# Optimization experiments

Measured on AMD Instinct MI355X. Metric: run time of the kernel, lower is better.

The kernel has to match this reference:

```python
import jax, jax.numpy as jnp
import numpy as np

N_NODES = 100000
N_EDGES = 1600000
IN, HID, OUT = 128, 128, 64


def setup_inputs() -> dict:
    key = jax.random.key(0)
    ks = jax.random.split(key, 12)
    x = jax.random.normal(ks[0], (N_NODES, IN), dtype=jnp.float32)
    src = jax.random.randint(ks[1], (N_EDGES,), 0, N_NODES, dtype=jnp.int32)
    dst = jax.random.randint(ks[2], (N_EDGES,), 0, N_NODES, dtype=jnp.int32)

    def lin(k, fan_in, fan_out):
        return jax.random.normal(k, (fan_in, fan_out), dtype=jnp.float32) / jnp.sqrt(jnp.float32(fan_in))

    return {
        "x": x, "src": src, "dst": dst,
        "w_self_0": lin(ks[3], IN, HID), "w_neigh_0": lin(ks[4], IN, HID), "b_0": jnp.zeros((HID,), jnp.float32),
        "w_self_1": lin(ks[5], HID, HID), "w_neigh_1": lin(ks[6], HID, HID), "b_1": jnp.zeros((HID,), jnp.float32),
        "w_self_2": lin(ks[7], HID, OUT), "w_neigh_2": lin(ks[8], HID, OUT), "b_2": jnp.zeros((OUT,), jnp.float32),
    }


def reference(x, src, dst, w_self_0, w_neigh_0, b_0, w_self_1, w_neigh_1, b_1, w_self_2, w_neigh_2, b_2):
    n = x.shape[0]
    # in-degree per dst node; zero-degree nodes keep aggregated 0 (clamp avoids div-by-0)
    deg = jax.ops.segment_sum(jnp.ones_like(dst, dtype=x.dtype), dst, num_segments=n)
    inv_deg = (1.0 / jnp.maximum(deg, 1.0))[:, None]

    def sage_layer(h, w_s, w_n, b):
        # irregular gather of src features, segment-mean over dst
        agg = jax.ops.segment_sum(h[src], dst, num_segments=n) * inv_deg
        return h @ w_s + agg @ w_n + b

    h = jax.nn.relu(sage_layer(x, w_self_0, w_neigh_0, b_0))   # dropout = identity (eval)
    h = jax.nn.relu(sage_layer(h, w_self_1, w_neigh_1, b_1))
    return sage_layer(h, w_self_2, w_neigh_2, b_2)
```

## Files before the change

### kernel.cpp

```cpp
#include <hip/hip_runtime.h>


#define NN 100000
#define NE 1600000
#define BSH 7
#define BND 128
#define NB  782
#define NBLKS 256
#define EPB ((NE + NBLKS - 1) / NBLKS)
#define STOT (NB * NBLKS)
#define NSB ((STOT + 1023) / 1024)
#define GEMM_BLOCKS 1563

typedef __attribute__((ext_vector_type(8))) short short8;
typedef __attribute__((ext_vector_type(4))) float f32x4;
typedef unsigned int uint;
typedef unsigned short ushort;

__device__ inline ushort f2bf(float f) {
    uint u = __float_as_uint(f);
    u += 0x7FFFu + ((u >> 16) & 1u);
    return (ushort)(u >> 16);
}
__device__ inline float bf_lo(uint w) { return __uint_as_float(w << 16); }
__device__ inline float bf_hi(uint w) { return __uint_as_float(w & 0xFFFF0000u); }

template<int NCS, int NCN, bool XF32, bool ABF>
__device__ void gemm_body(int bid, int tid,
    const void* __restrict__ Hv, const ushort* __restrict__ Wf,
    const float* __restrict__ bias, void* __restrict__ Av, ushort* __restrict__ Bt)
{
    constexpr int NCT = (NCS + NCN) / 16;
    const int g = (bid * 256 + tid) >> 6;
    if (g >= NN / 16) return;
    const int lane = tid & 63;
    const int m = lane & 15;
    const int q = lane >> 4;

    short8 af[4];
    if (XF32) {
        const float* hp = (const float*)Hv + (size_t)(g * 16 + m) * 128;
        #pragma unroll
        for (int kt = 0; kt < 4; ++kt) {
            const float4 f0 = *(const float4*)(hp + kt * 32 + q * 8);
            const float4 f1 = *(const float4*)(hp + kt * 32 + q * 8 + 4);
            short8 v;
            v[0] = (short)f2bf(f0.x); v[1] = (short)f2bf(f0.y);
            v[2] = (short)f2bf(f0.z); v[3] = (short)f2bf(f0.w);
            v[4] = (short)f2bf(f1.x); v[5] = (short)f2bf(f1.y);
            v[6] = (short)f2bf(f1.z); v[7] = (short)f2bf(f1.w);
            af[kt] = v;
        }
    } else {
        const short8* hp = (const short8*)((const ushort*)Hv + (size_t)(g * 16 + m) * 128);
        #pragma unroll
        for (int kt = 0; kt < 4; ++kt) af[kt] = hp[kt * 4 + q];
    }

    f32x4 acc[NCT];
    #pragma unroll
    for (int i = 0; i < NCT; ++i) acc[i] = (f32x4){0.f, 0.f, 0.f, 0.f};

    const short8* wp = (const short8*)Wf;
    #pragma unroll
    for (int ct = 0; ct < NCT; ++ct) {
        #pragma unroll
        for (int kt = 0; kt < 4; ++kt) {
            const short8 bf = wp[(ct * 4 + kt) * 64 + lane];
            acc[ct] = __builtin_amdgcn_mfma_f32_16x16x32_bf16(af[kt], bf, acc[ct], 0, 0, 0);
        }
    }

    const int r0 = g * 16 + q * 4;
    #pragma unroll
    for (int ct = 0; ct < NCS / 16; ++ct) {
        const int c = ct * 16 + m;
        const float bv = bias[c];
        #pragma unroll
        for (int r = 0; r < 4; ++r) {
            const float v = acc[ct][r] + bv;
            if (ABF) ((ushort*)Av)[(size_t)(r0 + r) * NCS + c] = f2bf(v);
            else     ((float*) Av)[(size_t)(r0 + r) * NCS + c] = v;
        }
    }
    #pragma unroll
    for (int ct = NCS / 16; ct < NCT; ++ct) {
        const int c = ct * 16 + m - NCS;
        #pragma unroll
        for (int r = 0; r < 4; ++r)
            Bt[(size_t)(r0 + r) * NCN + c] = f2bf(acc[ct][r]);
    }
}

template<int NCS, int NCN, bool XF32, bool ABF>
__global__ __launch_bounds__(256) void gemm_mfma_k(
    const void* __restrict__ Hv, const ushort* __restrict__ Wf,
    const float* __restrict__ bias, void* __restrict__ Av, ushort* __restrict__ Bt)
{
    gemm_body<NCS, NCN, XF32, ABF>(blockIdx.x, threadIdx.x, Hv, Wf, bias, Av, Bt);
}

__global__ __launch_bounds__(256) void phist_pack_k(
    const int* __restrict__ dst, int* __restrict__ histG,
    const float* __restrict__ ws0, const float* __restrict__ wn0, ushort* __restrict__ wf0,
    const float* __restrict__ ws1, const float* __restrict__ wn1, ushort* __restrict__ wf1,
    const float* __restrict__ ws2, const float* __restrict__ wn2, ushort* __restrict__ wf2)
{
    __shared__ int h[NB];
    const int t = threadIdx.x;
    if (blockIdx.x < NBLKS) {
        for (int i = t; i < NB; i += 256) h[i] = 0;
        __syncthreads();
        const int blk = blockIdx.x;
        const int e0 = blk * EPB;
        const int e1 = min(e0 + EPB, NE);
        for (int e = e0 + t; e < e1; e += 256)
            atomicAdd(&h[dst[e] >> BSH], 1);
        __syncthreads();
        for (int i = t; i < NB; i += 256)
            histG[i * NBLKS + blk] = h[i];
        return;
    }
    const int b = blockIdx.x - NBLKS;
    const float *ws, *wn; ushort* wf; int ncs, idx;
    if (b < 16)      { ws = ws0; wn = wn0; wf = wf0; ncs = 128; idx = b * 256 + t; }
    else if (b < 32) { ws = ws1; wn = wn1; wf = wf1; ncs = 128; idx = (b - 16) * 256 + t; }
    else             { ws = ws2; wn = wn2; wf = wf2; ncs = 64;  idx = (b - 32) * 256 + t; }
    const int total = (2 * ncs / 16) * 4 * 64;
    if (idx >= total) return;
    const int l = idx & 63;
    const int f = idx >> 6;
    const int kt = f & 3;
    const int ct = f >> 2;
    const int n = ct * 16 + (l & 15);
    const int k0 = kt * 32 + (l >> 4) * 8;
    uint w[4];
    #pragma unroll
    for (int p = 0; p < 4; ++p) {
        const int k = k0 + p * 2;
        float v0, v1;
        if (n < ncs) { v0 = ws[k * ncs + n];         v1 = ws[(k + 1) * ncs + n]; }
        else         { v0 = wn[k * ncs + (n - ncs)]; v1 = wn[(k + 1) * ncs + (n - ncs)]; }
        w[p] = (uint)f2bf(v0) | ((uint)f2bf(v1) << 16);
    }
    uint4 o; o.x = w[0]; o.y = w[1]; o.z = w[2]; o.w = w[3];
    ((uint4*)wf)[idx] = o;
}

__global__ __launch_bounds__(256) void scan1_k(int* __restrict__ data, int* __restrict__ blksum) {
    __shared__ int lds[256];
    const int t = threadIdx.x;
    const int base = blockIdx.x * 1024 + t * 4;
    int v[4];
    #pragma unroll
    for (int i = 0; i < 4; ++i) {
        const int idx = base + i;
        v[i] = (idx < STOT) ? data[idx] : 0;
    }
    const int s = v[0] + v[1] + v[2] + v[3];
    lds[t] = s;
    __syncthreads();
    #pragma unroll
    for (int off = 1; off < 256; off <<= 1) {
        const int cur = lds[t];
        const int y = (t >= off) ? lds[t - off] : 0;
        __syncthreads();
        lds[t] = cur + y;
        __syncthreads();
    }
    const int incl = lds[t];
    if (t == 255) blksum[blockIdx.x] = incl;
    int run = incl - s;
    #pragma unroll
    for (int i = 0; i < 4; ++i) {
        const int idx = base + i;
        if (idx < STOT) data[idx] = run;
        run += v[i];
    }
}

__global__ __launch_bounds__(256) void scan3_k(int* __restrict__ data, const int* __restrict__ blksum) {
    __shared__ int lds[256];
    const int t = threadIdx.x;
    lds[t] = (t < NSB) ? blksum[t] : 0;
    __syncthreads();
    #pragma unroll
    for (int off = 1; off < 256; off <<= 1) {
        const int cur = lds[t];
        const int y = (t >= off) ? lds[t - off] : 0;
        __syncthreads();
        lds[t] = cur + y;
        __syncthreads();
    }
    const int add = (blockIdx.x == 0) ? 0 : lds[blockIdx.x - 1];
    const int base = blockIdx.x * 1024 + t * 4;
    #pragma unroll
    for (int i = 0; i < 4; ++i) {
        const int idx = base + i;
        if (idx < STOT) data[idx] += add;
    }
}

__global__ __launch_bounds__(256) void pscatter_gemm0_k(
    const int* __restrict__ src, const int* __restrict__ dst,
    const int* __restrict__ histG, int* __restrict__ pb,
    const float* __restrict__ x, const ushort* __restrict__ wf0,
    const float* __restrict__ b0, ushort* __restrict__ Abf, ushort* __restrict__ Bt)
{
    __shared__ int wc[NB];
    const int t = threadIdx.x;
    if (blockIdx.x < NBLKS) {
        const int blk = blockIdx.x;
        for (int i = t; i < NB; i += 256) wc[i] = histG[i * NBLKS + blk];
        __syncthreads();
        const int e0 = blk * EPB;
        const int e1 = min(e0 + EPB, NE);
        for (int e = e0 + t; e < e1; e += 256) {
            const int d = dst[e];
            const int pos = atomicAdd(&wc[d >> BSH], 1);
            pb[pos] = (src[e] << BSH) | (d & (BND - 1));
        }
        return;
    }
    gemm_body<128, 128, true, true>(blockIdx.x - NBLKS, t, x, wf0, b0, Abf, Bt);
}

__global__ __launch_bounds__(256) void bucket_place_k(const int* __restrict__ histG,
                                                      const int* __restrict__ pb,
                                                      int* __restrict__ row,
                                                      int* __restrict__ esrc) {
    __shared__ int cnt[BND], wc[BND], excl[BND], scan[BND];
    const int b = blockIdx.x;
    const int t = threadIdx.x;
    if (t < BND) { cnt[t] = 0; wc[t] = 0; }
    __syncthreads();
    const int s0 = histG[b * NBLKS];
    const int s1 = (b + 1 < NB) ? histG[(b + 1) * NBLKS] : NE;
    for (int e = s0 + t; e < s1; e += 256)
        atomicAdd(&cnt[pb[e] & (BND - 1)], 1);
    __syncthreads();
    if (t < BND) scan[t] = cnt[t];
    __syncthreads();
    for (int off = 1; off < BND; off <<= 1) {
        int nv = 0;
        if (t < BND) {
            nv = scan[t];
            if (t >= off) nv += scan[t - off];
        }
        __syncthreads();
        if (t < BND) scan[t] = nv;
        __syncthreads();
    }
    if (t < BND) {
        const int ex = scan[t] - cnt[t];
        excl[t] = ex;
        const int node = b * BND + t;
        if (node <= NN) row[node] = s0 + ex;
    }
    __syncthreads();
    for (int e = s0 + t; e < s1; e += 256) {
        const int p = pb[e];
        const int dl = p & (BND - 1);
        const int pos = s0 + excl[dl] + atomicAdd(&wc[dl], 1);
        esrc[pos] = p >> BSH;
    }
}

__global__ __launch_bounds__(256) void agg128_k(
    const int* __restrict__ row, const int* __restrict__ esrc,
    const ushort* __restrict__ Bt, const ushort* __restrict__ Abf, ushort* __restrict__ Hb)
{
    const int w = (blockIdx.x * 256 + threadIdx.x) >> 6;
    const int half = (threadIdx.x >> 5) & 1;
    const int ln = threadIdx.x & 31;
    const int node = w * 2 + half;
    if (node >= NN) return;
    const int e0 = row[node];
    const int e1 = row[node + 1];
    const uint2* B = (const uint2*)Bt;
    float a0 = 0.f, a1 = 0.f, a2 = 0.f, a3 = 0.f;
    int e = e0;
    for (; e + 8 <= e1; e += 8) {
        int s[8];
        #pragma unroll
        for (int j = 0; j < 8; ++j) s[j] = esrc[e + j];
        uint2 v[8];
        #pragma unroll
        for (int j = 0; j < 8; ++j) v[j] = B[(size_t)s[j] * 32 + ln];
        #pragma unroll
        for (int j = 0; j < 8; ++j) {
            a0 += bf_lo(v[j].x); a1 += bf_hi(v[j].x);
            a2 += bf_lo(v[j].y); a3 += bf_hi(v[j].y);
        }
    }
    for (; e + 2 <= e1; e += 2) {
        const int s0 = esrc[e], s1 = esrc[e + 1];
        const uint2 v0 = B[(size_t)s0 * 32 + ln];
        const uint2 v1 = B[(size_t)s1 * 32 + ln];
        a0 += bf_lo(v0.x) + bf_lo(v1.x); a1 += bf_hi(v0.x) + bf_hi(v1.x);
        a2 += bf_lo(v0.y) + bf_lo(v1.y); a3 += bf_hi(v0.y) + bf_hi(v1.y);
    }
    if (e < e1) {
        const uint2 v = B[(size_t)esrc[e] * 32 + ln];
        a0 += bf_lo(v.x); a1 += bf_hi(v.x);
        a2 += bf_lo(v.y); a3 += bf_hi(v.y);
    }
    const int deg = e1 - e0;
    const float invd = (deg > 0) ? 1.0f / (float)deg : 0.0f;
    const uint2 aw = ((const uint2*)Abf)[(size_t)node * 32 + ln];
    const float v0 = fmaxf(bf_lo(aw.x) + a0 * invd, 0.f);
    const float v1 = fmaxf(bf_hi(aw.x) + a1 * invd, 0.f);
    const float v2 = fmaxf(bf_lo(aw.y) + a2 * invd, 0.f);
    const float v3 = fmaxf(bf_hi(aw.y) + a3 * invd, 0.f);
    uint2 o;
    o.x = (uint)f2bf(v0) | ((uint)f2bf(v1) << 16);
    o.y = (uint)f2bf(v2) | ((uint)f2bf(v3) << 16);
    ((uint2*)Hb)[(size_t)node * 32 + ln] = o;
}

__global__ __launch_bounds__(256) void agg64_k(
    const int* __restrict__ row, const int* __restrict__ esrc,
    const ushort* __restrict__ Bt, float* __restrict__ out)
{
    const int node = (blockIdx.x * 256 + threadIdx.x) >> 4;
    const int ln = threadIdx.x & 15;
    if (node >= NN) return;
    const int e0 = row[node];
    const int e1 = row[node + 1];
    const uint2* B = (const uint2*)Bt;
    float a0 = 0.f, a1 = 0.f, a2 = 0.f, a3 = 0.f;
    int e = e0;
    for (; e + 8 <= e1; e += 8) {
        int s[8];
        #pragma unroll
        for (int j = 0; j < 8; ++j) s[j] = esrc[e + j];
        uint2 v[8];
        #pragma unroll
        for (int j = 0; j < 8; ++j) v[j] = B[(size_t)s[j] * 16 + ln];
        #pragma unroll
        for (int j = 0; j < 8; ++j) {
            a0 += bf_lo(v[j].x); a1 += bf_hi(v[j].x);
            a2 += bf_lo(v[j].y); a3 += bf_hi(v[j].y);
        }
    }
    for (; e + 2 <= e1; e += 2) {
        const int s0 = esrc[e], s1 = esrc[e + 1];
        const uint2 v0 = B[(size_t)s0 * 16 + ln];
        const uint2 v1 = B[(size_t)s1 * 16 + ln];
        a0 += bf_lo(v0.x) + bf_lo(v1.x); a1 += bf_hi(v0.x) + bf_hi(v1.x);
        a2 += bf_lo(v0.y) + bf_lo(v1.y); a3 += bf_hi(v0.y) + bf_hi(v1.y);
    }
    if (e < e1) {
        const uint2 v = B[(size_t)esrc[e] * 16 + ln];
        a0 += bf_lo(v.x); a1 += bf_hi(v.x);
        a2 += bf_lo(v.y); a3 += bf_hi(v.y);
    }
    const int deg = e1 - e0;
    const float invd = (deg > 0) ? 1.0f / (float)deg : 0.0f;
    float4* op = (float4*)(out + (size_t)node * 64 + ln * 4);
    float4 o = *op;
    o.x += a0 * invd; o.y += a1 * invd;
    o.z += a2 * invd; o.w += a3 * invd;
    *op = o;
}

__device__ inline float4 relu4f(float4 v) {
    v.x = fmaxf(v.x, 0.f); v.y = fmaxf(v.y, 0.f);
    v.z = fmaxf(v.z, 0.f); v.w = fmaxf(v.w, 0.f);
    return v;
}
template<int NCOL, bool RELU_IN, bool BIAS>
__global__ __launch_bounds__(256) void gemm_k(
    const float* in, const float* __restrict__ W,
    const float* __restrict__ bias, float* out)
{
    constexpr int K = 128;
    constexpr int QUADS = NCOL / 4;
    constexpr int G = 256 / QUADS;
    constexpr int RPT = 32 / G;
    __shared__ float Wlds[K * NCOL];
    {
        const float4* Wg = reinterpret_cast<const float4*>(W);
        float4* Wl = reinterpret_cast<float4*>(Wlds);
        #pragma unroll
        for (int i = 0; i < K * NCOL / 4 / 256; ++i)
            Wl[threadIdx.x + i * 256] = Wg[threadIdx.x + i * 256];
    }
    __syncthreads();
    const int tx = threadIdx.x % QUADS;
    const int ty = threadIdx.x / QUADS;
    const int row0 = blockIdx.x * 32;
    const float* rp[RPT];
    #pragma unroll
    for (int i = 0; i < RPT; ++i) rp[i] = in + (size_t)(row0 + ty + i * G) * K;
    float acc[RPT][4];
    #pragma unroll
    for (int i = 0; i < RPT; ++i) acc[i][0] = acc[i][1] = acc[i][2] = acc[i][3] = 0.f;
    #pragma unroll 2
    for (int kc = 0; kc < K; kc += 4) {
        float4 h4[RPT];
        #pragma unroll
        for (int i = 0; i < RPT; ++i) {
            h4[i] = *reinterpret_cast<const float4*>(rp[i] + kc);
            if (RELU_IN) h4[i] = relu4f(h4[i]);
        }
        #pragma unroll
        for (int kk = 0; kk < 4; ++kk) {
            const float4 w4 = *reinterpret_cast<const float4*>(&Wlds[(kc + kk) * NCOL + tx * 4]);
            #pragma unroll
            for (int i = 0; i < RPT; ++i) {
                const float hv = (&h4[i].x)[kk];
                acc[i][0] = fmaf(hv, w4.x, acc[i][0]);
                acc[i][1] = fmaf(hv, w4.y, acc[i][1]);
                acc[i][2] = fmaf(hv, w4.z, acc[i][2]);
                acc[i][3] = fmaf(hv, w4.w, acc[i][3]);
            }
        }
    }
    float4 b4 = make_float4(0.f, 0.f, 0.f, 0.f);
    if (BIAS) b4 = *reinterpret_cast<const float4*>(&bias[tx * 4]);
    #pragma unroll
    for (int i = 0; i < RPT; ++i) {
        const int r = row0 + ty + i * G;
        float4 o;
        o.x = acc[i][0] + b4.x; o.y = acc[i][1] + b4.y;
        o.z = acc[i][2] + b4.z; o.w = acc[i][3] + b4.w;
        *reinterpret_cast<float4*>(&out[(size_t)r * NCOL + tx * 4]) = o;
    }
}
__global__ void deg_k(const int* __restrict__ dst, float* __restrict__ deg, int E) {
    const int i = blockIdx.x * blockDim.x + threadIdx.x;
    if (i < E) atomicAdd(&deg[dst[i]], 1.0f);
}
__global__ void inv_k(float* deg, int n) {
    const int i = blockIdx.x * blockDim.x + threadIdx.x;
    if (i < n) deg[i] = 1.0f / fmaxf(deg[i], 1.0f);
}
__global__ __launch_bounds__(256) void scatter128_k(
    const int* __restrict__ src, const int* __restrict__ dst,
    const float* __restrict__ inv, const float* __restrict__ B, float* A, int E) {
    const int lane = threadIdx.x & 63;
    int w = (blockIdx.x * 256 + threadIdx.x) >> 6;
    const int nw = (gridDim.x * 256) >> 6;
    for (int e = w; e < E; e += nw) {
        const int s = src[e], d = dst[e];
        const float sc = inv[d];
        const float2 v = *reinterpret_cast<const float2*>(&B[(size_t)s * 128 + lane * 2]);
        atomicAdd(&A[(size_t)d * 128 + lane * 2    ], v.x * sc);
        atomicAdd(&A[(size_t)d * 128 + lane * 2 + 1], v.y * sc);
    }
}
__global__ __launch_bounds__(256) void scatter64_k(
    const int* __restrict__ src, const int* __restrict__ dst,
    const float* __restrict__ inv, const float* __restrict__ B, float* A, int E) {
    const int lane = threadIdx.x & 63;
    int w = (blockIdx.x * 256 + threadIdx.x) >> 6;
    const int nw = (gridDim.x * 256) >> 6;
    for (int e = w; e < E; e += nw) {
        const int s = src[e], d = dst[e];
        atomicAdd(&A[(size_t)d * 64 + lane], B[(size_t)s * 64 + lane] * inv[d]);
    }
}

extern "C" void kernel_launch(void* const* d_in, const int* in_sizes, int n_in,
                              void* d_out, int out_size, void* d_ws, size_t ws_size,
                              hipStream_t stream) {
    const float* x   = (const float*)d_in[0];
    const int*   src = (const int*)  d_in[1];
    const int*   dst = (const int*)  d_in[2];
    const float* ws0 = (const float*)d_in[3];
    const float* wn0 = (const float*)d_in[4];
    const float* b0  = (const float*)d_in[5];
    const float* ws1 = (const float*)d_in[6];
    const float* wn1 = (const float*)d_in[7];
    const float* b1  = (const float*)d_in[8];
    const float* ws2 = (const float*)d_in[9];
    const float* wn2 = (const float*)d_in[10];
    const float* b2  = (const float*)d_in[11];
    float* out = (float*)d_out;

    const size_t O_BLK  = 4096;
    const size_t O_ROW  = 16384;
    const size_t O_WF0  = 417792;
    const size_t O_WF1  = 483328;
    const size_t O_WF2  = 548864;
    const size_t O_ESRC = 581632;
    const size_t O_PB   = 6983680;
    const size_t O_HIST = 13385728;
    const size_t O_A    = 14286848;
    const size_t O_BT   = 39890944;
    const size_t O_HB   = 65495040;
    const size_t NEED   = 91095040;

    if (ws_size >= NEED) {
        int*    blks  = (int*)   ((char*)d_ws + O_BLK);
        int*    row   = (int*)   ((char*)d_ws + O_ROW);
        ushort* wf0   = (ushort*)((char*)d_ws + O_WF0);
        ushort* wf1   = (ushort*)((char*)d_ws + O_WF1);
        ushort* wf2   = (ushort*)((char*)d_ws + O_WF2);
        int*    esrc  = (int*)   ((char*)d_ws + O_ESRC);
        int*    pb    = (int*)   ((char*)d_ws + O_PB);
        int*    histG = (int*)   ((char*)d_ws + O_HIST);
        ushort* Abf   = (ushort*)((char*)d_ws + O_A);
        ushort* Bt    = (ushort*)((char*)d_ws + O_BT);
        ushort* Hb    = (ushort*)((char*)d_ws + O_HB);

        phist_pack_k<<<NBLKS + 40, 256, 0, stream>>>(dst, histG,
            ws0, wn0, wf0, ws1, wn1, wf1, ws2, wn2, wf2);
        scan1_k<<<NSB, 256, 0, stream>>>(histG, blks);
        scan3_k<<<NSB, 256, 0, stream>>>(histG, blks);
        pscatter_gemm0_k<<<NBLKS + GEMM_BLOCKS, 256, 0, stream>>>(
            src, dst, histG, pb, x, wf0, b0, Abf, Bt);
        bucket_place_k<<<NB, 256, 0, stream>>>(histG, pb, row, esrc);

        const int AGG128_BLOCKS = (NN / 2 + 3) / 4;
        const int AGG64_BLOCKS  = (NN + 63) / 64;
        const int A64B = (NN + 15) / 16;

        agg128_k<<<AGG128_BLOCKS, 256, 0, stream>>>(row, esrc, Bt, Abf, Hb);
        gemm_mfma_k<128, 128, false, true ><<<GEMM_BLOCKS, 256, 0, stream>>>(Hb, wf1, b1, Abf, Bt);
        agg128_k<<<AGG128_BLOCKS, 256, 0, stream>>>(row, esrc, Bt, Abf, Hb);
        gemm_mfma_k<64, 64, false, false><<<GEMM_BLOCKS, 256, 0, stream>>>(Hb, wf2, b2, out, Bt);
        agg64_k<<<A64B, 256, 0, stream>>>(row, esrc, Bt, out);
        (void)AGG64_BLOCKS;
    } else {
        float* inv = (float*)d_ws;
        float* H0  = (float*)((char*)d_ws + (1u << 20));
        float* Bf  = H0 + (size_t)NN * 128;
        const int GB = NN / 32;
        const int SC_BLOCKS = 4096;
        hipMemsetAsync(inv, 0, NN * sizeof(float), stream);
        deg_k<<<(NE + 255) / 256, 256, 0, stream>>>(dst, inv, NE);
        inv_k<<<(NN + 255) / 256, 256, 0, stream>>>(inv, NN);
        gemm_k<128, false, false><<<GB, 256, 0, stream>>>(x, wn0, nullptr, Bf);
        gemm_k<128, false, true ><<<GB, 256, 0, stream>>>(x, ws0, b0, H0);
        scatter128_k<<<SC_BLOCKS, 256, 0, stream>>>(src, dst, inv, Bf, H0, NE);
        gemm_k<128, true, false><<<GB, 256, 0, stream>>>(H0, wn1, nullptr, Bf);
        gemm_k<128, true, true ><<<GB, 256, 0, stream>>>(H0, ws1, b1, H0);
        scatter128_k<<<SC_BLOCKS, 256, 0, stream>>>(src, dst, inv, Bf, H0, NE);
        gemm_k<64, true, false><<<GB, 256, 0, stream>>>(H0, wn2, nullptr, Bf);
        gemm_k<64, true, true ><<<GB, 256, 0, stream>>>(H0, ws2, b2, out);
        scatter64_k<<<SC_BLOCKS, 256, 0, stream>>>(src, dst, inv, Bf, out, NE);
    }
}
```

Measured before the change: 397.5 us.

## Slice feature layout for aggregation and fold bucket scan into scatter kernel

Stores intermediate bf16 feature matrices in a column-sliced layout (16 features per slice, node-major within a slice), so each aggregation block gathers only a 32-byte slice per neighbor, with the blockIdx-interleaved slice order intended to keep each slice's working set cache-resident. Aggregation now splits edges across 8 lane groups and reduces with shuffles. The global histogram plus two scan kernels are replaced by a per-block local scan inside the scatter kernel, with bucket totals accumulated via atomics and prefix-summed inside bucket_place. The change trades fewer launches and better cache locality for more aggregation blocks, shuffle reductions, and a serial per-thread loop in bucket placement.

```diff
diff --git a/kernel.cpp b/kernel.cpp
--- a/kernel.cpp
+++ b/kernel.cpp
@@ -7,9 +7,7 @@
 #define BND 128
 #define NB  782
 #define NBLKS 256
-#define EPB ((NE + NBLKS - 1) / NBLKS)
-#define STOT (NB * NBLKS)
-#define NSB ((STOT + 1023) / 1024)
+#define EPB (NE / NBLKS)
 #define GEMM_BLOCKS 1563
 
 typedef __attribute__((ext_vector_type(8))) short short8;
@@ -25,103 +23,13 @@
 __device__ inline float bf_lo(uint w) { return __uint_as_float(w << 16); }
 __device__ inline float bf_hi(uint w) { return __uint_as_float(w & 0xFFFF0000u); }
 
-template<int NCS, int NCN, bool XF32, bool ABF>
-__device__ void gemm_body(int bid, int tid,
-    const void* __restrict__ Hv, const ushort* __restrict__ Wf,
-    const float* __restrict__ bias, void* __restrict__ Av, ushort* __restrict__ Bt)
-{
-    constexpr int NCT = (NCS + NCN) / 16;
-    const int g = (bid * 256 + tid) >> 6;
-    if (g >= NN / 16) return;
-    const int lane = tid & 63;
-    const int m = lane & 15;
-    const int q = lane >> 4;
-
-    short8 af[4];
-    if (XF32) {
-        const float* hp = (const float*)Hv + (size_t)(g * 16 + m) * 128;
-        #pragma unroll
-        for (int kt = 0; kt < 4; ++kt) {
-            const float4 f0 = *(const float4*)(hp + kt * 32 + q * 8);
-            const float4 f1 = *(const float4*)(hp + kt * 32 + q * 8 + 4);
-            short8 v;
-            v[0] = (short)f2bf(f0.x); v[1] = (short)f2bf(f0.y);
-            v[2] = (short)f2bf(f0.z); v[3] = (short)f2bf(f0.w);
-            v[4] = (short)f2bf(f1.x); v[5] = (short)f2bf(f1.y);
-            v[6] = (short)f2bf(f1.z); v[7] = (short)f2bf(f1.w);
-            af[kt] = v;
-        }
-    } else {
-        const short8* hp = (const short8*)((const ushort*)Hv + (size_t)(g * 16 + m) * 128);
-        #pragma unroll
-        for (int kt = 0; kt < 4; ++kt) af[kt] = hp[kt * 4 + q];
-    }
-
-    f32x4 acc[NCT];
-    #pragma unroll
-    for (int i = 0; i < NCT; ++i) acc[i] = (f32x4){0.f, 0.f, 0.f, 0.f};
-
-    const short8* wp = (const short8*)Wf;
-    #pragma unroll
-    for (int ct = 0; ct < NCT; ++ct) {
-        #pragma unroll
-        for (int kt = 0; kt < 4; ++kt) {
-            const short8 bf = wp[(ct * 4 + kt) * 64 + lane];
-            acc[ct] = __builtin_amdgcn_mfma_f32_16x16x32_bf16(af[kt], bf, acc[ct], 0, 0, 0);
-        }
-    }
-
-    const int r0 = g * 16 + q * 4;
-    #pragma unroll
-    for (int ct = 0; ct < NCS / 16; ++ct) {
-        const int c = ct * 16 + m;
-        const float bv = bias[c];
-        #pragma unroll
-        for (int r = 0; r < 4; ++r) {
-            const float v = acc[ct][r] + bv;
-            if (ABF) ((ushort*)Av)[(size_t)(r0 + r) * NCS + c] = f2bf(v);
-            else     ((float*) Av)[(size_t)(r0 + r) * NCS + c] = v;
-        }
-    }
-    #pragma unroll
-    for (int ct = NCS / 16; ct < NCT; ++ct) {
-        const int c = ct * 16 + m - NCS;
-        #pragma unroll
-        for (int r = 0; r < 4; ++r)
-            Bt[(size_t)(r0 + r) * NCN + c] = f2bf(acc[ct][r]);
-    }
-}
-
-template<int NCS, int NCN, bool XF32, bool ABF>
-__global__ __launch_bounds__(256) void gemm_mfma_k(
-    const void* __restrict__ Hv, const ushort* __restrict__ Wf,
-    const float* __restrict__ bias, void* __restrict__ Av, ushort* __restrict__ Bt)
-{
-    gemm_body<NCS, NCN, XF32, ABF>(blockIdx.x, threadIdx.x, Hv, Wf, bias, Av, Bt);
-}
-
-__global__ __launch_bounds__(256) void phist_pack_k(
-    const int* __restrict__ dst, int* __restrict__ histG,
+__global__ __launch_bounds__(256) void pack_k(
     const float* __restrict__ ws0, const float* __restrict__ wn0, ushort* __restrict__ wf0,
     const float* __restrict__ ws1, const float* __restrict__ wn1, ushort* __restrict__ wf1,
     const float* __restrict__ ws2, const float* __restrict__ wn2, ushort* __restrict__ wf2)
 {
-    __shared__ int h[NB];
+    const int b = blockIdx.x;
     const int t = threadIdx.x;
-    if (blockIdx.x < NBLKS) {
-        for (int i = t; i < NB; i += 256) h[i] = 0;
-        __syncthreads();
-        const int blk = blockIdx.x;
-        const int e0 = blk * EPB;
-        const int e1 = min(e0 + EPB, NE);
-        for (int e = e0 + t; e < e1; e += 256)
-            atomicAdd(&h[dst[e] >> BSH], 1);
-        __syncthreads();
-        for (int i = t; i < NB; i += 256)
-            histG[i * NBLKS + blk] = h[i];
-        return;
-    }
-    const int b = blockIdx.x - NBLKS;
     const float *ws, *wn; ushort* wf; int ncs, idx;
     if (b < 16)      { ws = ws0; wn = wn0; wf = wf0; ncs = 128; idx = b * 256 + t; }
     else if (b < 32) { ws = ws1; wn = wn1; wf = wf1; ncs = 128; idx = (b - 16) * 256 + t; }
@@ -147,97 +55,170 @@
     ((uint4*)wf)[idx] = o;
 }
 
-__global__ __launch_bounds__(256) void scan1_k(int* __restrict__ data, int* __restrict__ blksum) {
-    __shared__ int lds[256];
-    const int t = threadIdx.x;
-    const int base = blockIdx.x * 1024 + t * 4;
-    int v[4];
-    #pragma unroll
-    for (int i = 0; i < 4; ++i) {
-        const int idx = base + i;
-        v[i] = (idx < STOT) ? data[idx] : 0;
-    }
-    const int s = v[0] + v[1] + v[2] + v[3];
-    lds[t] = s;
-    __syncthreads();
-    #pragma unroll
-    for (int off = 1; off < 256; off <<= 1) {
-        const int cur = lds[t];
-        const int y = (t >= off) ? lds[t - off] : 0;
-        __syncthreads();
-        lds[t] = cur + y;
-        __syncthreads();
-    }
-    const int incl = lds[t];
-    if (t == 255) blksum[blockIdx.x] = incl;
-    int run = incl - s;
-    #pragma unroll
-    for (int i = 0; i < 4; ++i) {
-        const int idx = base + i;
-        if (idx < STOT) data[idx] = run;
-        run += v[i];
-    }
-}
-
-__global__ __launch_bounds__(256) void scan3_k(int* __restrict__ data, const int* __restrict__ blksum) {
-    __shared__ int lds[256];
-    const int t = threadIdx.x;
-    lds[t] = (t < NSB) ? blksum[t] : 0;
-    __syncthreads();
-    #pragma unroll
-    for (int off = 1; off < 256; off <<= 1) {
-        const int cur = lds[t];
-        const int y = (t >= off) ? lds[t - off] : 0;
-        __syncthreads();
-        lds[t] = cur + y;
-        __syncthreads();
-    }
-    const int add = (blockIdx.x == 0) ? 0 : lds[blockIdx.x - 1];
-    const int base = blockIdx.x * 1024 + t * 4;
-    #pragma unroll
-    for (int i = 0; i < 4; ++i) {
-        const int idx = base + i;
-        if (idx < STOT) data[idx] += add;
-    }
+template<int NCS, int NCN, bool XF32, bool ABF>
+__device__ void gemm_body(int bid, int tid,
+    const void* __restrict__ Hv, const ushort* __restrict__ Wf,
+    const float* __restrict__ bias, void* __restrict__ Av, ushort* __restrict__ Bt)
+{
+    constexpr int NCT = (NCS + NCN) / 16;
+    const int g = (bid * 256 + tid) >> 6;
+    if (g >= NN / 16) return;
+    const int lane = tid & 63;
+    const int m = lane & 15;
+    const int q = lane >> 4;
+    const int node = g * 16 + m;
+
+    short8 af[4];
+    if (XF32) {
+        const float* hp = (const float*)Hv + (size_t)node * 128;
+        #pragma unroll
+        for (int kt = 0; kt < 4; ++kt) {
+            const float4 f0 = *(const float4*)(hp + kt * 32 + q * 8);
+            const float4 f1 = *(const float4*)(hp + kt * 32 + q * 8 + 4);
+            short8 v;
+            v[0] = (short)f2bf(f0.x); v[1] = (short)f2bf(f0.y);
+            v[2] = (short)f2bf(f0.z); v[3] = (short)f2bf(f0.w);
+            v[4] = (short)f2bf(f1.x); v[5] = (short)f2bf(f1.y);
+            v[6] = (short)f2bf(f1.z); v[7] = (short)f2bf(f1.w);
+            af[kt] = v;
+        }
+    } else {
+        const ushort* Hs = (const ushort*)Hv;
+        #pragma unroll
+        for (int kt = 0; kt < 4; ++kt) {
+            const int sl = 2 * kt + (q >> 1);
+            af[kt] = *(const short8*)(Hs + (size_t)sl * NN * 16 + (size_t)node * 16 + 8 * (q & 1));
+        }
+    }
+
+    f32x4 acc[NCT];
+    #pragma unroll
+    for (int i = 0; i < NCT; ++i) acc[i] = (f32x4){0.f, 0.f, 0.f, 0.f};
+
+    const short8* wp = (const short8*)Wf;
+    #pragma unroll
+    for (int ct = 0; ct < NCT; ++ct) {
+        #pragma unroll
+        for (int kt = 0; kt < 4; ++kt) {
+            const short8 bf = wp[(ct * 4 + kt) * 64 + lane];
+            acc[ct] = __builtin_amdgcn_mfma_f32_16x16x32_bf16(af[kt], bf, acc[ct], 0, 0, 0);
+        }
+    }
+
+    const int r0 = g * 16 + q * 4;
+    #pragma unroll
+    for (int ct = 0; ct < NCS / 16; ++ct) {
+        const int c = ct * 16 + m;
+        const float bv = bias[c];
+        #pragma unroll
+        for (int r = 0; r < 4; ++r) {
+            const float v = acc[ct][r] + bv;
+            if (ABF) ((ushort*)Av)[(size_t)ct * NN * 16 + (size_t)(r0 + r) * 16 + m] = f2bf(v);
+            else     ((float*) Av)[(size_t)(r0 + r) * NCS + c] = v;
+        }
+    }
+    #pragma unroll
+    for (int ct = NCS / 16; ct < NCT; ++ct) {
+        const int s = ct - NCS / 16;
+        #pragma unroll
+        for (int r = 0; r < 4; ++r)
+            Bt[(size_t)s * NN * 16 + (size_t)(r0 + r) * 16 + m] = f2bf(acc[ct][r]);
+    }
+}
+
+template<int NCS, int NCN, bool XF32, bool ABF>
+__global__ __launch_bounds__(256) void gemm_mfma_k(
+    const void* __restrict__ Hv, const ushort* __restrict__ Wf,
+    const float* __restrict__ bias, void* __restrict__ Av, ushort* __restrict__ Bt)
+{
+    gemm_body<NCS, NCN, XF32, ABF>(blockIdx.x, threadIdx.x, Hv, Wf, bias, Av, Bt);
 }
 
 __global__ __launch_bounds__(256) void pscatter_gemm0_k(
     const int* __restrict__ src, const int* __restrict__ dst,
-    const int* __restrict__ histG, int* __restrict__ pb,
+    int* __restrict__ pb, int* __restrict__ lofs, int* __restrict__ btot,
     const float* __restrict__ x, const ushort* __restrict__ wf0,
     const float* __restrict__ b0, ushort* __restrict__ Abf, ushort* __restrict__ Bt)
 {
+    __shared__ int h[NB];
     __shared__ int wc[NB];
+    __shared__ int tsum[256];
     const int t = threadIdx.x;
-    if (blockIdx.x < NBLKS) {
-        const int blk = blockIdx.x;
-        for (int i = t; i < NB; i += 256) wc[i] = histG[i * NBLKS + blk];
+    if (blockIdx.x >= NBLKS) {
+        gemm_body<128, 128, true, true>(blockIdx.x - NBLKS, t, x, wf0, b0, Abf, Bt);
+        return;
+    }
+    const int blk = blockIdx.x;
+    const int e0 = blk * EPB;
+    for (int i = t; i < NB; i += 256) h[i] = 0;
+    __syncthreads();
+    for (int e = e0 + t; e < e0 + EPB; e += 256)
+        atomicAdd(&h[dst[e] >> BSH], 1);
+    __syncthreads();
+    int v[4];
+    const int base4 = t * 4;
+    #pragma unroll
+    for (int i = 0; i < 4; ++i) {
+        const int idx = base4 + i;
+        v[i] = (idx < NB) ? h[idx] : 0;
+    }
+    const int s = v[0] + v[1] + v[2] + v[3];
+    tsum[t] = s;
+    __syncthreads();
+    #pragma unroll
+    for (int off = 1; off < 256; off <<= 1) {
+        const int cur = tsum[t];
+        const int y = (t >= off) ? tsum[t - off] : 0;
         __syncthreads();
-        const int e0 = blk * EPB;
-        const int e1 = min(e0 + EPB, NE);
-        for (int e = e0 + t; e < e1; e += 256) {
-            const int d = dst[e];
-            const int pos = atomicAdd(&wc[d >> BSH], 1);
-            pb[pos] = (src[e] << BSH) | (d & (BND - 1));
-        }
-        return;
-    }
-    gemm_body<128, 128, true, true>(blockIdx.x - NBLKS, t, x, wf0, b0, Abf, Bt);
-}
-
-__global__ __launch_bounds__(256) void bucket_place_k(const int* __restrict__ histG,
-                                                      const int* __restrict__ pb,
-                                                      int* __restrict__ row,
-                                                      int* __restrict__ esrc) {
+        tsum[t] = cur + y;
+        __syncthreads();
+    }
+    int run = tsum[t] - s;
+    #pragma unroll
+    for (int i = 0; i < 4; ++i) {
+        const int idx = base4 + i;
+        if (idx < NB) {
+            wc[idx] = run;
+            lofs[idx * NBLKS + blk] = run;
+            if (v[i]) atomicAdd(&btot[idx], v[i]);
+        }
+        run += v[i];
+    }
+    __syncthreads();
+    for (int e = e0 + t; e < e0 + EPB; e += 256) {
+        const int d = dst[e];
+        const int pos = e0 + atomicAdd(&wc[d >> BSH], 1);
+        pb[pos] = (src[e] << BSH) | (d & (BND - 1));
+    }
+}
+
+__global__ __launch_bounds__(256) void bucket_place_k(
+    const int* __restrict__ btot, const int* __restrict__ lofs,
+    const int* __restrict__ pb, int* __restrict__ row, int* __restrict__ esrc)
+{
     __shared__ int cnt[BND], wc[BND], excl[BND], scan[BND];
+    __shared__ int red[256];
     const int b = blockIdx.x;
     const int t = threadIdx.x;
+    int part = 0;
+    #pragma unroll
+    for (int i = 0; i < 4; ++i) {
+        const int idx = t * 4 + i;
+        if (idx < b && idx < NB) part += btot[idx];
+    }
+    red[t] = part;
     if (t < BND) { cnt[t] = 0; wc[t] = 0; }
     __syncthreads();
-    const int s0 = histG[b * NBLKS];
-    const int s1 = (b + 1 < NB) ? histG[(b + 1) * NBLKS] : NE;
-    for (int e = s0 + t; e < s1; e += 256)
-        atomicAdd(&cnt[pb[e] & (BND - 1)], 1);
+    for (int off = 128; off > 0; off >>= 1) {
+        if (t < off) red[t] += red[t + off];
+        __syncthreads();
+    }
+    const int s0 = red[0];
+    const int lo = lofs[b * NBLKS + t];
+    const int lcount = ((b + 1 < NB) ? lofs[(b + 1) * NBLKS + t] : EPB) - lo;
+    const int lstart = t * EPB + lo;
+    for (int k = 0; k < lcount; ++k)
+        atomicAdd(&cnt[pb[lstart + k] & (BND - 1)], 1);
     __syncthreads();
     if (t < BND) scan[t] = cnt[t];
     __syncthreads();
@@ -258,8 +239,8 @@
         if (node <= NN) row[node] = s0 + ex;
     }
     __syncthreads();
-    for (int e = s0 + t; e < s1; e += 256) {
-        const int p = pb[e];
+    for (int k = 0; k < lcount; ++k) {
+        const int p = pb[lstart + k];
         const int dl = p & (BND - 1);
         const int pos = s0 + excl[dl] + atomicAdd(&wc[dl], 1);
         esrc[pos] = p >> BSH;
@@ -268,100 +249,86 @@
 
 __global__ __launch_bounds__(256) void agg128_k(
     const int* __restrict__ row, const int* __restrict__ esrc,
-    const ushort* __restrict__ Bt, const ushort* __restrict__ Abf, ushort* __restrict__ Hb)
-{
-    const int w = (blockIdx.x * 256 + threadIdx.x) >> 6;
-    const int half = (threadIdx.x >> 5) & 1;
-    const int ln = threadIdx.x & 31;
-    const int node = w * 2 + half;
-    if (node >= NN) return;
+    const uint* __restrict__ BtU, const uint* __restrict__ AbfU, uint* __restrict__ HbU)
+{
+    const int slice = blockIdx.x & 7;
+    const int node = (blockIdx.x >> 3) * 4 + (threadIdx.x >> 6);
+    const int lane = threadIdx.x & 63;
+    const int f = lane & 7;
+    const int g = lane >> 3;
     const int e0 = row[node];
     const int e1 = row[node + 1];
-    const uint2* B = (const uint2*)Bt;
-    float a0 = 0.f, a1 = 0.f, a2 = 0.f, a3 = 0.f;
-    int e = e0;
-    for (; e + 8 <= e1; e += 8) {
-        int s[8];
-        #pragma unroll
-        for (int j = 0; j < 8; ++j) s[j] = esrc[e + j];
-        uint2 v[8];
-        #pragma unroll
-        for (int j = 0; j < 8; ++j) v[j] = B[(size_t)s[j] * 32 + ln];
-        #pragma unroll
-        for (int j = 0; j < 8; ++j) {
-            a0 += bf_lo(v[j].x); a1 += bf_hi(v[j].x);
-            a2 += bf_lo(v[j].y); a3 += bf_hi(v[j].y);
-        }
-    }
-    for (; e + 2 <= e1; e += 2) {
-        const int s0 = esrc[e], s1 = esrc[e + 1];
-        const uint2 v0 = B[(size_t)s0 * 32 + ln];
-        const uint2 v1 = B[(size_t)s1 * 32 + ln];
-        a0 += bf_lo(v0.x) + bf_lo(v1.x); a1 += bf_hi(v0.x) + bf_hi(v1.x);
-        a2 += bf_lo(v0.y) + bf_lo(v1.y); a3 += bf_hi(v0.y) + bf_hi(v1.y);
+    const uint* B = BtU + (size_t)slice * NN * 8;
+    float a0 = 0.f, a1 = 0.f;
+    int e = e0 + g;
+    for (; e + 8 < e1; e += 16) {
+        const int s0 = __builtin_nontemporal_load(esrc + e);
+        const int s1 = __builtin_nontemporal_load(esrc + e + 8);
+        const uint v0 = B[(size_t)s0 * 8 + f];
+        const uint v1 = B[(size_t)s1 * 8 + f];
+        a0 += bf_lo(v0) + bf_lo(v1);
+        a1 += bf_hi(v0) + bf_hi(v1);
     }
     if (e < e1) {
-        const uint2 v = B[(size_t)esrc[e] * 32 + ln];
-        a0 += bf_lo(v.x); a1 += bf_hi(v.x);
-        a2 += bf_lo(v.y); a3 += bf_hi(v.y);
-    }
-    const int deg = e1 - e0;
-    const float invd = (deg > 0) ? 1.0f / (float)deg : 0.0f;
-    const uint2 aw = ((const uint2*)Abf)[(size_t)node * 32 + ln];
-    const float v0 = fmaxf(bf_lo(aw.x) + a0 * invd, 0.f);
-    const float v1 = fmaxf(bf_hi(aw.x) + a1 * invd, 0.f);
-    const float v2 = fmaxf(bf_lo(aw.y) + a2 * invd, 0.f);
-    const float v3 = fmaxf(bf_hi(aw.y) + a3 * invd, 0.f);
-    uint2 o;
-    o.x = (uint)f2bf(v0) | ((uint)f2bf(v1) << 16);
-    o.y = (uint)f2bf(v2) | ((uint)f2bf(v3) << 16);
-    ((uint2*)Hb)[(size_t)node * 32 + ln] = o;
+        const int s0 = __builtin_nontemporal_load(esrc + e);
+        const uint v0 = B[(size_t)s0 * 8 + f];
+        a0 += bf_lo(v0);
+        a1 += bf_hi(v0);
+    }
+    a0 += __shfl_xor(a0, 8);  a1 += __shfl_xor(a1, 8);
+    a0 += __shfl_xor(a0, 16); a1 += __shfl_xor(a1, 16);
+    a0 += __shfl_xor(a0, 32); a1 += __shfl_xor(a1, 32);
+    if (g == 0) {
+        const int deg = e1 - e0;
+        const float invd = (deg > 0) ? 1.0f / (float)deg : 0.0f;
+        const uint aw = __builtin_nontemporal_load(AbfU + (size_t)slice * NN * 8 + (size_t)node * 8 + f);
+        const float v0 = fmaxf(bf_lo(aw) + a0 * invd, 0.f);
+        const float v1 = fmaxf(bf_hi(aw) + a1 * invd, 0.f);
+        __builtin_nontemporal_store((uint)f2bf(v0) | ((uint)f2bf(v1) << 16),
+                                    HbU + (size_t)slice * NN * 8 + (size_t)node * 8 + f);
+    }
 }
 
 __global__ __launch_bounds__(256) void agg64_k(
     const int* __restrict__ row, const int* __restrict__ esrc,
-    const ushort* __restrict__ Bt, float* __restrict__ out)
-{
-    const int node = (blockIdx.x * 256 + threadIdx.x) >> 4;
-    const int ln = threadIdx.x & 15;
-    if (node >= NN) return;
+    const uint* __restrict__ BtU, float* __restrict__ out)
+{
+    const int slice = blockIdx.x & 3;
+    const int node = (blockIdx.x >> 2) * 4 + (threadIdx.x >> 6);
+    const int lane = threadIdx.x & 63;
+    const int f = lane & 7;
+    const int g = lane >> 3;
     const int e0 = row[node];
     const int e1 = row[node + 1];
-    const uint2* B = (const uint2*)Bt;
-    float a0 = 0.f, a1 = 0.f, a2 = 0.f, a3 = 0.f;
-    int e = e0;
-    for (; e + 8 <= e1; e += 8) {
-        int s[8];
-        #pragma unroll
-        for (int j = 0; j < 8; ++j) s[j] = esrc[e + j];
-        uint2 v[8];
-        #pragma unroll
-        for (int j = 0; j < 8; ++j) v[j] = B[(size_t)s[j] * 16 + ln];
-        #pragma unroll
-        for (int j = 0; j < 8; ++j) {
-            a0 += bf_lo(v[j].x); a1 += bf_hi(v[j].x);
-            a2 += bf_lo(v[j].y); a3 += bf_hi(v[j].y);
-        }
-    }
-    for (; e + 2 <= e1; e += 2) {
-        const int s0 = esrc[e], s1 = esrc[e + 1];
-        const uint2 v0 = B[(size_t)s0 * 16 + ln];
-        const uint2 v1 = B[(size_t)s1 * 16 + ln];
-        a0 += bf_lo(v0.x) + bf_lo(v1.x); a1 += bf_hi(v0.x) + bf_hi(v1.x);
-        a2 += bf_lo(v0.y) + bf_lo(v1.y); a3 += bf_hi(v0.y) + bf_hi(v1.y);
+    const uint* B = BtU + (size_t)slice * NN * 8;
+    float a0 = 0.f, a1 = 0.f;
+    int e = e0 + g;
+    for (; e + 8 < e1; e += 16) {
+        const int s0 = __builtin_nontemporal_load(esrc + e);
+        const int s1 = __builtin_nontemporal_load(esrc + e + 8);
+        const uint v0 = B[(size_t)s0 * 8 + f];
+        const uint v1 = B[(size_t)s1 * 8 + f];
+        a0 += bf_lo(v0) + bf_lo(v1);
+        a1 += bf_hi(v0) + bf_hi(v1);
     }
     if (e < e1) {
-        const uint2 v = B[(size_t)esrc[e] * 16 + ln];
-        a0 += bf_lo(v.x); a1 += bf_hi(v.x);
-        a2 += bf_lo(v.y); a3 += bf_hi(v.y);
-    }
-    const int deg = e1 - e0;
-    const float invd = (deg > 0) ? 1.0f / (float)deg : 0.0f;
-    float4* op = (float4*)(out + (size_t)node * 64 + ln * 4);
-    float4 o = *op;
-    o.x += a0 * invd; o.y += a1 * invd;
-    o.z += a2 * invd; o.w += a3 * invd;
-    *op = o;
+        const int s0 = __builtin_nontemporal_load(esrc + e);
+        const uint v0 = B[(size_t)s0 * 8 + f];
+        a0 += bf_lo(v0);
+        a1 += bf_hi(v0);
+    }
+    a0 += __shfl_xor(a0, 8);  a1 += __shfl_xor(a1, 8);
+    a0 += __shfl_xor(a0, 16); a1 += __shfl_xor(a1, 16);
+    a0 += __shfl_xor(a0, 32); a1 += __shfl_xor(a1, 32);
+    if (g == 0) {
+        const int deg = e1 - e0;
+        const float invd = (deg > 0) ? 1.0f / (float)deg : 0.0f;
+        float2* op = (float2*)(out + (size_t)node * 64 + slice * 16 + f * 2);
+        float2 o = *op;
+        o.x += a0 * invd;
+        o.y += a1 * invd;
+        *op = o;
+    }
 }
 
 __device__ inline float4 relu4f(float4 v) {
@@ -479,50 +446,46 @@
     const float* b2  = (const float*)d_in[11];
     float* out = (float*)d_out;
 
-    const size_t O_BLK  = 4096;
+    const size_t O_BTOT = 4096;
     const size_t O_ROW  = 16384;
     const size_t O_WF0  = 417792;
     const size_t O_WF1  = 483328;
     const size_t O_WF2  = 548864;
     const size_t O_ESRC = 581632;
     const size_t O_PB   = 6983680;
-    const size_t O_HIST = 13385728;
-    const size_t O_A    = 14286848;
-    const size_t O_BT   = 39890944;
-    const size_t O_HB   = 65495040;
-    const size_t NEED   = 91095040;
+    const size_t O_LOFS = 13383680;
+    const size_t O_A    = 14185472;
+    const size_t O_BT   = 39785472;
+    const size_t O_HB   = 65385472;
+    const size_t NEED   = 90985472;
 
     if (ws_size >= NEED) {
-        int*    blks  = (int*)   ((char*)d_ws + O_BLK);
-        int*    row   = (int*)   ((char*)d_ws + O_ROW);
-        ushort* wf0   = (ushort*)((char*)d_ws + O_WF0);
-        ushort* wf1   = (ushort*)((char*)d_ws + O_WF1);
-        ushort* wf2   = (ushort*)((char*)d_ws + O_WF2);
-        int*    esrc  = (int*)   ((char*)d_ws + O_ESRC);
-        int*    pb    = (int*)   ((char*)d_ws + O_PB);
-        int*    histG = (int*)   ((char*)d_ws + O_HIST);
-        ushort* Abf   = (ushort*)((char*)d_ws + O_A);
-        ushort* Bt    = (ushort*)((char*)d_ws + O_BT);
-        ushort* Hb    = (ushort*)((char*)d_ws + O_HB);
-
-        phist_pack_k<<<NBLKS + 40, 256, 0, stream>>>(dst, histG,
-            ws0, wn0, wf0, ws1, wn1, wf1, ws2, wn2, wf2);
-        scan1_k<<<NSB, 256, 0, stream>>>(histG, blks);
-        scan3_k<<<NSB, 256, 0, stream>>>(histG, blks);
+        int*    btot = (int*)   ((char*)d_ws + O_BTOT);
+        int*    row  = (int*)   ((char*)d_ws + O_ROW);
+        ushort* wf0  = (ushort*)((char*)d_ws + O_WF0);
+        ushort* wf1  = (ushort*)((char*)d_ws + O_WF1);
+        ushort* wf2  = (ushort*)((char*)d_ws + O_WF2);
+        int*    esrc = (int*)   ((char*)d_ws + O_ESRC);
+        int*    pb   = (int*)   ((char*)d_ws + O_PB);
+        int*    lofs = (int*)   ((char*)d_ws + O_LOFS);
+        ushort* Abf  = (ushort*)((char*)d_ws + O_A);
+        ushort* Bt   = (ushort*)((char*)d_ws + O_BT);
+        ushort* Hb   = (ushort*)((char*)d_ws + O_HB);
+
+        hipMemsetAsync(btot, 0, NB * sizeof(int), stream);
+        pack_k<<<40, 256, 0, stream>>>(ws0, wn0, wf0, ws1, wn1, wf1, ws2, wn2, wf2);
         pscatter_gemm0_k<<<NBLKS + GEMM_BLOCKS, 256, 0, stream>>>(
-            src, dst, histG, pb, x, wf0, b0, Abf, Bt);
-        bucket_place_k<<<NB, 256, 0, stream>>>(histG, pb, row, esrc);
-
-        const int AGG128_BLOCKS = (NN / 2 + 3) / 4;
-        const int AGG64_BLOCKS  = (NN + 63) / 64;
-        const int A64B = (NN + 15) / 16;
-
-        agg128_k<<<AGG128_BLOCKS, 256, 0, stream>>>(row, esrc, Bt, Abf, Hb);
+            src, dst, pb, lofs, btot, x, wf0, b0, Abf, Bt);
+        bucket_place_k<<<NB, 256, 0, stream>>>(btot, lofs, pb, row, esrc);
+
+        const int AGG128_GRID = 8 * (NN / 4);
+        const int AGG64_GRID  = 4 * (NN / 4);
+
+        agg128_k<<<AGG128_GRID, 256, 0, stream>>>(row, esrc, (uint*)Bt, (uint*)Abf, (uint*)Hb);
         gemm_mfma_k<128, 128, false, true ><<<GEMM_BLOCKS, 256, 0, stream>>>(Hb, wf1, b1, Abf, Bt);
-        agg128_k<<<AGG128_BLOCKS, 256, 0, stream>>>(row, esrc, Bt, Abf, Hb);
+        agg128_k<<<AGG128_GRID, 256, 0, stream>>>(row, esrc, (uint*)Bt, (uint*)Abf, (uint*)Hb);
         gemm_mfma_k<64, 64, false, false><<<GEMM_BLOCKS, 256, 0, stream>>>(Hb, wf2, b2, out, Bt);
-        agg64_k<<<A64B, 256, 0, stream>>>(row, esrc, Bt, out);
-        (void)AGG64_BLOCKS;
+        agg64_k<<<AGG64_GRID, 256, 0, stream>>>(row, esrc, (uint*)Bt, out);
     } else {
         float* inv = (float*)d_ws;
         float* H0  = (float*)((char*)d_ws + (1u << 20));
```

New measurement: 898.6 us. 2.26x slower.
